# Performance work log

Hardware: AMD Instinct MI355X
Metric: run time of the kernel (lower is better)

## Reference

```python
import jax, jax.numpy as jnp
import numpy as np

NUM_NODES = 8192
IN_FEATURES = 1024
OUT_FEATURES = 512
NUM_EDGES = 262144  # avg degree 32


def setup_inputs() -> dict:
    key = jax.random.key(0)
    k_x, k_w, k_b, k_src, k_dst = jax.random.split(key, 5)
    x = jax.random.normal(k_x, (NUM_NODES, IN_FEATURES), dtype=jnp.float32)
    # torch nn.Linear layout: weight [out, in], bias [out]
    W = jax.random.normal(k_w, (OUT_FEATURES, IN_FEATURES), dtype=jnp.float32) * (1.0 / np.sqrt(IN_FEATURES))
    b = jax.random.normal(k_b, (OUT_FEATURES,), dtype=jnp.float32) * 0.01
    src = jax.random.randint(k_src, (NUM_EDGES,), 0, NUM_NODES, dtype=jnp.int64)
    dst = jax.random.randint(k_dst, (NUM_EDGES,), 0, NUM_NODES, dtype=jnp.int64)
    edge_index = jnp.stack([src, dst], axis=0)
    return {"x": x, "W": W, "b": b, "edge_index": edge_index, "num_nodes": NUM_NODES}


def reference(x, W, b, edge_index, num_nodes):
    # Faithful to the torch module: build dense adjacency from edge list
    # (duplicate edges collapse to 1.0 via assignment semantics),
    # linear, (dropout p=0 -> identity), dense adj @ hidden, relu.
    adj = jnp.zeros((num_nodes, num_nodes), dtype=x.dtype)
    adj = adj.at[edge_index[0], edge_index[1]].set(1.0)
    hidden = x @ W.T + b            # [N, out]
    support = adj @ hidden          # [N, out] aggregation over neighbors
    return jax.nn.relu(support)
```

## Files before the change

kernel.cpp:

```cpp
#include <hip/hip_runtime.h>

#define N_NODES 8192
#define IN_F    1024
#define OUT_F   512
#define N_EDGES 262144
#define STRIDE  96

#define HID_OFF     0u
#define XB_OFF      8388608u
#define WB_OFF      25165824u
#define DEG_OFF     26214400u
#define COL_OFF     26247168u
#define UCNT_OFF    29392896u
#define UCOL_OFF    29425664u
#define MAX_DEG     STRIDE

typedef short  bf16x8 __attribute__((ext_vector_type(8)));
typedef float  f32x4  __attribute__((ext_vector_type(4)));
typedef float  f32x2  __attribute__((ext_vector_type(2)));

__device__ __forceinline__ unsigned short f2bf(float f) {
    unsigned u = __float_as_uint(f);
    u += 0x7fffu + ((u >> 16) & 1u);
    return (unsigned short)(u >> 16);
}

__device__ __forceinline__ float bflo(unsigned u) { return __uint_as_float(u << 16); }
__device__ __forceinline__ float bfhi(unsigned u) { return __uint_as_float(u & 0xffff0000u); }

__device__ __forceinline__ void ld_lds16(const void* g, void* l) {
    __builtin_amdgcn_global_load_lds(
        (const __attribute__((address_space(1))) void*)g,
        (__attribute__((address_space(3))) void*)l, 16, 0, 0);
}

#define NX8 (N_NODES * IN_F / 8)
#define NW8 (OUT_F * IN_F / 8)
__global__ __launch_bounds__(256) void cvt_bf16_all(const float* __restrict__ x,
                                                    const float* __restrict__ w,
                                                    unsigned short* __restrict__ xb,
                                                    int* __restrict__ deg) {
    int i = blockIdx.x * blockDim.x + threadIdx.x;
    if (i < N_NODES) deg[i] = 0;
    if (i >= NX8 + NW8) return;
    const f32x4* p = (i < NX8) ? ((const f32x4*)x + (size_t)i * 2)
                               : ((const f32x4*)w + (size_t)(i - NX8) * 2);
    f32x4 v0 = __builtin_nontemporal_load(p);
    f32x4 v1 = __builtin_nontemporal_load(p + 1);
    uint4 o;
    o.x = (unsigned)f2bf(v0.x) | ((unsigned)f2bf(v0.y) << 16);
    o.y = (unsigned)f2bf(v0.z) | ((unsigned)f2bf(v0.w) << 16);
    o.z = (unsigned)f2bf(v1.x) | ((unsigned)f2bf(v1.y) << 16);
    o.w = (unsigned)f2bf(v1.z) | ((unsigned)f2bf(v1.w) << 16);
    *((uint4*)xb + i) = o;
}

#define GEMM_BLOCKS 512

__global__ __launch_bounds__(256, 2) void gemm_scatter(const unsigned short* __restrict__ Xb,
                                                       const unsigned short* __restrict__ Wb,
                                                       const float* __restrict__ bias,
                                                       unsigned short* __restrict__ H,
                                                       const int* __restrict__ src,
                                                       const int* __restrict__ dst,
                                                       int* __restrict__ deg,
                                                       int* __restrict__ col) {
    __shared__ unsigned short As[2][128 * 64];
    __shared__ unsigned short Bs[2][64 * 64];

    const int bid = blockIdx.x;
    const int tid = threadIdx.x;

    if (bid >= GEMM_BLOCKS) {
        int e = (bid - GEMM_BLOCKS) * 256 + tid;
        int s = src[e];
        int slot = atomicAdd(&deg[s], 1);
        if (slot < STRIDE) col[s * STRIDE + slot] = dst[e];
        return;
    }

    const int lane = tid & 63;
    const int wave = tid >> 6;
    const int row0 = (bid & 63) * 128;
    const int col0 = (bid >> 6) * 64;
    const int wm   = (wave & 1) * 64;
    const int wn   = (wave >> 1) * 32;
    const int fm   = lane & 15;
    const int fm7  = fm & 7;
    const int q    = lane >> 4;

    f32x4 acc[4][2];
#pragma unroll
    for (int i = 0; i < 4; ++i)
#pragma unroll
        for (int j = 0; j < 2; ++j) acc[i][j] = (f32x4)0.f;

    const int r0 = tid >> 3;
    const int kp = ((tid & 7) ^ (r0 & 7)) * 8;
    const unsigned short* Xbase = Xb + (size_t)(row0 + r0) * IN_F + kp;
    const unsigned short* Wbase = Wb + (size_t)(col0 + r0) * IN_F + kp;

#define STAGE(buf, k0) do {                                                   \
    ld_lds16(Xbase            + (k0), &As[buf][tid * 8]);                     \
    ld_lds16(Xbase + 32*IN_F  + (k0), &As[buf][(tid + 256) * 8]);             \
    ld_lds16(Xbase + 64*IN_F  + (k0), &As[buf][(tid + 512) * 8]);             \
    ld_lds16(Xbase + 96*IN_F  + (k0), &As[buf][(tid + 768) * 8]);             \
    ld_lds16(Wbase            + (k0), &Bs[buf][tid * 8]);                     \
    ld_lds16(Wbase + 32*IN_F  + (k0), &Bs[buf][(tid + 256) * 8]);             \
} while (0)

#define COMPUTE(buf) do {                                                     \
    _Pragma("unroll")                                                         \
    for (int s = 0; s < 2; ++s) {                                             \
        const int kq = s * 4 + q;                                             \
        bf16x8 a[4], b[2];                                                    \
        _Pragma("unroll")                                                     \
        for (int mi = 0; mi < 4; ++mi)                                        \
            a[mi] = *(const bf16x8*)&As[buf][(((wm + mi*16 + fm) << 3) + (kq ^ fm7)) << 3]; \
        _Pragma("unroll")                                                     \
        for (int ni = 0; ni < 2; ++ni)                                        \
            b[ni] = *(const bf16x8*)&Bs[buf][(((wn + ni*16 + fm) << 3) + (kq ^ fm7)) << 3]; \
        _Pragma("unroll")                                                     \
        for (int mi = 0; mi < 4; ++mi)                                        \
            _Pragma("unroll")                                                 \
            for (int ni = 0; ni < 2; ++ni)                                    \
                acc[mi][ni] = __builtin_amdgcn_mfma_f32_16x16x32_bf16(        \
                    a[mi], b[ni], acc[mi][ni], 0, 0, 0);                      \
    }                                                                         \
} while (0)

    STAGE(0, 0);
    __syncthreads();
    int cur = 0;
    for (int t = 0; t < 15; ++t) {
        STAGE(cur ^ 1, (t + 1) * 64);
        COMPUTE(cur);
        __syncthreads();
        cur ^= 1;
    }
    COMPUTE(cur);

    const int cm = (lane >> 4) * 4;
#pragma unroll
    for (int ni = 0; ni < 2; ++ni) {
        const int c = col0 + wn + ni * 16 + fm;
        const float bv = bias[c];
#pragma unroll
        for (int mi = 0; mi < 4; ++mi) {
#pragma unroll
            for (int r = 0; r < 4; ++r) {
                const int row = row0 + wm + mi * 16 + cm + r;
                H[(size_t)row * OUT_F + c] = f2bf(acc[mi][ni][r] + bv);
            }
        }
    }
#undef STAGE
#undef COMPUTE
}

__global__ __launch_bounds__(256) void dedup(const int* __restrict__ dg,
                                             const int* __restrict__ col,
                                             int* __restrict__ ucol,
                                             int* __restrict__ ucnt) {
    __shared__ int nbr[4][MAX_DEG];
    __shared__ int wcnt[4];
    const int wave = threadIdx.x >> 6;
    const int lane = threadIdx.x & 63;
    const int v    = blockIdx.x * 4 + wave;
    int d = dg[v];
    if (d > MAX_DEG) d = MAX_DEG;

    if (lane == 0) wcnt[wave] = 0;
    int id0 = -1, id1 = -1;
    if (lane < d)      { id0 = col[v * STRIDE + lane];      nbr[wave][lane]      = id0; }
    if (64 + lane < d) { id1 = col[v * STRIDE + 64 + lane]; nbr[wave][64 + lane] = id1; }
    __builtin_amdgcn_wave_barrier();

    bool k0 = (lane < d);
    const int lim0 = k0 ? lane : 0;
    for (int j = 0; j < lim0; ++j) k0 = k0 & (nbr[wave][j] != id0);
    bool k1 = (64 + lane < d);
    const int lim1 = k1 ? (64 + lane) : 0;
    for (int j = 0; j < lim1; ++j) k1 = k1 & (nbr[wave][j] != id1);
    if (k0) ucol[v * STRIDE + atomicAdd(&wcnt[wave], 1)] = id0;
    if (k1) ucol[v * STRIDE + atomicAdd(&wcnt[wave], 1)] = id1;
    __builtin_amdgcn_wave_barrier();
    if (lane == 0) ucnt[v] = wcnt[wave];
}

__global__ __launch_bounds__(256, 8) void aggregate(const unsigned short* __restrict__ H,
                                                    const int* __restrict__ ucnt,
                                                    const int* __restrict__ ucol,
                                                    float* __restrict__ out) {
    const int wave = threadIdx.x >> 6;
    const int lane = threadIdx.x & 63;
    const int bid  = blockIdx.x;
    const int q    = bid & 3;
    const int v    = (bid >> 2) * 4 + wave;
    const int n    = ucnt[v];
    const int* uq  = ucol + v * STRIDE;
    const unsigned short* Hq = H + q * 128 + lane * 2;

    float a0 = 0.f, a1 = 0.f;
    int e = 0;
    for (; e + 16 <= n; e += 16) {
        unsigned h[16];
#pragma unroll
        for (int t = 0; t < 16; ++t)
            h[t] = *(const unsigned*)&Hq[(size_t)uq[e + t] * OUT_F];
#pragma unroll
        for (int t = 0; t < 16; ++t) { a0 += bflo(h[t]); a1 += bfhi(h[t]); }
    }
    for (; e + 4 <= n; e += 4) {
        unsigned h[4];
#pragma unroll
        for (int t = 0; t < 4; ++t)
            h[t] = *(const unsigned*)&Hq[(size_t)uq[e + t] * OUT_F];
#pragma unroll
        for (int t = 0; t < 4; ++t) { a0 += bflo(h[t]); a1 += bfhi(h[t]); }
    }
    for (; e < n; ++e) {
        unsigned h = *(const unsigned*)&Hq[(size_t)uq[e] * OUT_F];
        a0 += bflo(h); a1 += bfhi(h);
    }
    f32x2 o = {fmaxf(a0, 0.f), fmaxf(a1, 0.f)};
    __builtin_nontemporal_store(o, (f32x2*)&out[(size_t)v * OUT_F + q * 128 + lane * 2]);
}

extern "C" void kernel_launch(void* const* d_in, const int* in_sizes, int n_in,
                              void* d_out, int out_size, void* d_ws, size_t ws_size,
                              hipStream_t stream) {
    const float* x  = (const float*)d_in[0];
    const float* W  = (const float*)d_in[1];
    const float* b  = (const float*)d_in[2];
    const int*   ei = (const int*)d_in[3];
    float* out = (float*)d_out;

    char* ws = (char*)d_ws;
    unsigned short* H    = (unsigned short*)(ws + HID_OFF);
    unsigned short* Xb   = (unsigned short*)(ws + XB_OFF);
    unsigned short* Wb   = (unsigned short*)(ws + WB_OFF);
    int*            deg  = (int*)(ws + DEG_OFF);
    int*            col  = (int*)(ws + COL_OFF);
    int*            ucnt = (int*)(ws + UCNT_OFF);
    int*            ucol = (int*)(ws + UCOL_OFF);

    cvt_bf16_all<<<(NX8 + NW8 + 255) / 256, 256, 0, stream>>>(x, W, Xb, deg);

    gemm_scatter<<<GEMM_BLOCKS + N_EDGES / 256, 256, 0, stream>>>(
        Xb, Wb, b, H, ei, ei + N_EDGES, deg, col);

    dedup<<<N_NODES / 4, 256, 0, stream>>>(deg, col, ucol, ucnt);

    aggregate<<<N_NODES * 4 / 4, 256, 0, stream>>>(H, ucnt, ucol, out);
}
```

Before: 140.6 us.

## Fuse the X fp32-to-bf16 conversion into the GEMM LDS pipeline

Drops the separate pass that converted X to bf16 in global memory. The GEMM now streams fp32 X tiles straight into LDS through a swizzled layout and converts each A fragment to bf16 in registers with v_cvt_pk_bf16_f32 just before the MFMA. This removes a full read of fp32 X plus the write and re-read of the bf16 copy. In exchange, the A tile in LDS doubles in size, the GEMM moves twice as many bytes per X tile, and the conversion is repeated by every wave that shares those rows.

```diff
diff --git a/kernel.cpp b/kernel.cpp
--- a/kernel.cpp
+++ b/kernel.cpp
@@ -7,12 +7,11 @@
 #define STRIDE  96
 
 #define HID_OFF     0u
-#define XB_OFF      8388608u
-#define WB_OFF      25165824u
-#define DEG_OFF     26214400u
-#define COL_OFF     26247168u
-#define UCNT_OFF    29392896u
-#define UCOL_OFF    29425664u
+#define WB_OFF      8388608u
+#define DEG_OFF     9437184u
+#define COL_OFF     9469952u
+#define UCNT_OFF    12615680u
+#define UCOL_OFF    12648448u
 #define MAX_DEG     STRIDE
 
 typedef short  bf16x8 __attribute__((ext_vector_type(8)));
@@ -34,17 +33,13 @@
         (__attribute__((address_space(3))) void*)l, 16, 0, 0);
 }
 
-#define NX8 (N_NODES * IN_F / 8)
 #define NW8 (OUT_F * IN_F / 8)
-__global__ __launch_bounds__(256) void cvt_bf16_all(const float* __restrict__ x,
-                                                    const float* __restrict__ w,
-                                                    unsigned short* __restrict__ xb,
-                                                    int* __restrict__ deg) {
+__global__ __launch_bounds__(256) void cvt_w(const float* __restrict__ w,
+                                             unsigned short* __restrict__ wb,
+                                             int* __restrict__ deg) {
     int i = blockIdx.x * blockDim.x + threadIdx.x;
     if (i < N_NODES) deg[i] = 0;
-    if (i >= NX8 + NW8) return;
-    const f32x4* p = (i < NX8) ? ((const f32x4*)x + (size_t)i * 2)
-                               : ((const f32x4*)w + (size_t)(i - NX8) * 2);
+    const f32x4* p = (const f32x4*)w + (size_t)i * 2;
     f32x4 v0 = __builtin_nontemporal_load(p);
     f32x4 v1 = __builtin_nontemporal_load(p + 1);
     uint4 o;
@@ -52,12 +47,12 @@
     o.y = (unsigned)f2bf(v0.z) | ((unsigned)f2bf(v0.w) << 16);
     o.z = (unsigned)f2bf(v1.x) | ((unsigned)f2bf(v1.y) << 16);
     o.w = (unsigned)f2bf(v1.z) | ((unsigned)f2bf(v1.w) << 16);
-    *((uint4*)xb + i) = o;
+    *((uint4*)wb + i) = o;
 }
 
 #define GEMM_BLOCKS 512
 
-__global__ __launch_bounds__(256, 2) void gemm_scatter(const unsigned short* __restrict__ Xb,
+__global__ __launch_bounds__(256, 2) void gemm_scatter(const float* __restrict__ X,
                                                        const unsigned short* __restrict__ Wb,
                                                        const float* __restrict__ bias,
                                                        unsigned short* __restrict__ H,
@@ -65,7 +60,7 @@
                                                        const int* __restrict__ dst,
                                                        int* __restrict__ deg,
                                                        int* __restrict__ col) {
-    __shared__ unsigned short As[2][128 * 64];
+    __shared__ float          Asf[2][8192];
     __shared__ unsigned short Bs[2][64 * 64];
 
     const int bid = blockIdx.x;
@@ -95,28 +90,41 @@
 #pragma unroll
         for (int j = 0; j < 2; ++j) acc[i][j] = (f32x4)0.f;
 
+    const int acperm = (tid >> 1) & 7;
+    const int ac     = acperm ^ ((tid >> 4) & 7);
+    const float* Xa  = X + (size_t)(row0 + (tid >> 4)) * IN_F + ac * 8 + (tid & 1) * 4;
     const int r0 = tid >> 3;
     const int kp = ((tid & 7) ^ (r0 & 7)) * 8;
-    const unsigned short* Xbase = Xb + (size_t)(row0 + r0) * IN_F + kp;
     const unsigned short* Wbase = Wb + (size_t)(col0 + r0) * IN_F + kp;
 
 #define STAGE(buf, k0) do {                                                   \
-    ld_lds16(Xbase            + (k0), &As[buf][tid * 8]);                     \
-    ld_lds16(Xbase + 32*IN_F  + (k0), &As[buf][(tid + 256) * 8]);             \
-    ld_lds16(Xbase + 64*IN_F  + (k0), &As[buf][(tid + 512) * 8]);             \
-    ld_lds16(Xbase + 96*IN_F  + (k0), &As[buf][(tid + 768) * 8]);             \
+    _Pragma("unroll")                                                         \
+    for (int j = 0; j < 8; ++j)                                               \
+        ld_lds16(Xa + (size_t)j * 16 * IN_F + (k0),                           \
+                 &Asf[buf][(size_t)(j * 256 + tid) * 4]);                     \
     ld_lds16(Wbase            + (k0), &Bs[buf][tid * 8]);                     \
     ld_lds16(Wbase + 32*IN_F  + (k0), &Bs[buf][(tid + 256) * 8]);             \
 } while (0)
 
 #define COMPUTE(buf) do {                                                     \
     _Pragma("unroll")                                                         \
-    for (int s = 0; s < 2; ++s) {                                             \
-        const int kq = s * 4 + q;                                             \
+    for (int s2 = 0; s2 < 2; ++s2) {                                          \
+        const int kq = s2 * 4 + q;                                            \
         bf16x8 a[4], b[2];                                                    \
         _Pragma("unroll")                                                     \
-        for (int mi = 0; mi < 4; ++mi)                                        \
-            a[mi] = *(const bf16x8*)&As[buf][(((wm + mi*16 + fm) << 3) + (kq ^ fm7)) << 3]; \
+        for (int mi = 0; mi < 4; ++mi) {                                      \
+            const int rr = wm + mi * 16 + fm;                                 \
+            const f32x4* pa = (const f32x4*)&Asf[buf][(size_t)(rr * 16 + ((kq ^ fm7) << 1)) * 4]; \
+            f32x4 lo = pa[0], hi = pa[1];                                     \
+            unsigned u0, u1, u2, u3;                                          \
+            asm("v_cvt_pk_bf16_f32 %0, %1, %2" : "=v"(u0) : "v"(lo.x), "v"(lo.y)); \
+            asm("v_cvt_pk_bf16_f32 %0, %1, %2" : "=v"(u1) : "v"(lo.z), "v"(lo.w)); \
+            asm("v_cvt_pk_bf16_f32 %0, %1, %2" : "=v"(u2) : "v"(hi.x), "v"(hi.y)); \
+            asm("v_cvt_pk_bf16_f32 %0, %1, %2" : "=v"(u3) : "v"(hi.z), "v"(hi.w)); \
+            union { unsigned u[4]; bf16x8 v; } pk;                            \
+            pk.u[0] = u0; pk.u[1] = u1; pk.u[2] = u2; pk.u[3] = u3;           \
+            a[mi] = pk.v;                                                     \
+        }                                                                     \
         _Pragma("unroll")                                                     \
         for (int ni = 0; ni < 2; ++ni)                                        \
             b[ni] = *(const bf16x8*)&Bs[buf][(((wn + ni*16 + fm) << 3) + (kq ^ fm7)) << 3]; \
@@ -238,17 +246,16 @@
 
     char* ws = (char*)d_ws;
     unsigned short* H    = (unsigned short*)(ws + HID_OFF);
-    unsigned short* Xb   = (unsigned short*)(ws + XB_OFF);
     unsigned short* Wb   = (unsigned short*)(ws + WB_OFF);
     int*            deg  = (int*)(ws + DEG_OFF);
     int*            col  = (int*)(ws + COL_OFF);
     int*            ucnt = (int*)(ws + UCNT_OFF);
     int*            ucol = (int*)(ws + UCOL_OFF);
 
-    cvt_bf16_all<<<(NX8 + NW8 + 255) / 256, 256, 0, stream>>>(x, W, Xb, deg);
+    cvt_w<<<NW8 / 256, 256, 0, stream>>>(W, Wb, deg);
 
     gemm_scatter<<<GEMM_BLOCKS + N_EDGES / 256, 256, 0, stream>>>(
-        Xb, Wb, b, H, ei, ei + N_EDGES, deg, col);
+        x, Wb, b, H, ei, ei + N_EDGES, deg, col);
 
     dedup<<<N_NODES / 4, 256, 0, stream>>>(deg, col, ucol, ucnt);
 
```

Result: no change. 140.0 us (-0.4%).

## Reschedule graph preprocessing into conversion and GEMM kernels; widen GEMM tile to 128x128

Applied to the files above, without the earlier changes.

The edge scatter moves into the bf16 conversion kernel and the dedup pass moves into the GEMM kernel as extra blocks, with degree zeroing done by a memset. This removes one kernel launch and overlaps graph preprocessing with the dense work. The GEMM tile grows from 128x64 to 128x128, giving 256 blocks with more accumulators each. That raises register and LDS use per block and lowers the block count, which may hurt occupancy and load balance on the GPU's many CUs.

```diff
diff --git a/kernel.cpp b/kernel.cpp
--- a/kernel.cpp
+++ b/kernel.cpp
@@ -36,12 +36,23 @@
 
 #define NX8 (N_NODES * IN_F / 8)
 #define NW8 (OUT_F * IN_F / 8)
-__global__ __launch_bounds__(256) void cvt_bf16_all(const float* __restrict__ x,
-                                                    const float* __restrict__ w,
-                                                    unsigned short* __restrict__ xb,
-                                                    int* __restrict__ deg) {
-    int i = blockIdx.x * blockDim.x + threadIdx.x;
-    if (i < N_NODES) deg[i] = 0;
+#define SCAT_BLOCKS 1024
+__global__ __launch_bounds__(256) void cvt_scatter(const float* __restrict__ x,
+                                                   const float* __restrict__ w,
+                                                   unsigned short* __restrict__ xb,
+                                                   const int* __restrict__ src,
+                                                   const int* __restrict__ dst,
+                                                   int* __restrict__ deg,
+                                                   int* __restrict__ col) {
+    const int bid = blockIdx.x;
+    if (bid < SCAT_BLOCKS) {
+        int e = bid * 256 + threadIdx.x;
+        int s = src[e];
+        int slot = atomicAdd(&deg[s], 1);
+        if (slot < STRIDE) col[s * STRIDE + slot] = dst[e];
+        return;
+    }
+    int i = (bid - SCAT_BLOCKS) * 256 + threadIdx.x;
     if (i >= NX8 + NW8) return;
     const f32x4* p = (i < NX8) ? ((const f32x4*)x + (size_t)i * 2)
                                : ((const f32x4*)w + (size_t)(i - NX8) * 2);
@@ -55,75 +66,96 @@
     *((uint4*)xb + i) = o;
 }
 
-#define GEMM_BLOCKS 512
-
-__global__ __launch_bounds__(256, 2) void gemm_scatter(const unsigned short* __restrict__ Xb,
-                                                       const unsigned short* __restrict__ Wb,
-                                                       const float* __restrict__ bias,
-                                                       unsigned short* __restrict__ H,
-                                                       const int* __restrict__ src,
-                                                       const int* __restrict__ dst,
-                                                       int* __restrict__ deg,
-                                                       int* __restrict__ col) {
+#define GEMM_BLOCKS 256
+
+__global__ __launch_bounds__(256, 2) void gemm_dedup(const unsigned short* __restrict__ Xb,
+                                                     const unsigned short* __restrict__ Wb,
+                                                     const float* __restrict__ bias,
+                                                     unsigned short* __restrict__ H,
+                                                     const int* __restrict__ dg,
+                                                     const int* __restrict__ col,
+                                                     int* __restrict__ ucol,
+                                                     int* __restrict__ ucnt) {
     __shared__ unsigned short As[2][128 * 64];
-    __shared__ unsigned short Bs[2][64 * 64];
+    __shared__ unsigned short Bs[2][128 * 64];
+    __shared__ int wcnt[4];
 
     const int bid = blockIdx.x;
     const int tid = threadIdx.x;
-
-    if (bid >= GEMM_BLOCKS) {
-        int e = (bid - GEMM_BLOCKS) * 256 + tid;
-        int s = src[e];
-        int slot = atomicAdd(&deg[s], 1);
-        if (slot < STRIDE) col[s * STRIDE + slot] = dst[e];
-        return;
-    }
-
     const int lane = tid & 63;
     const int wave = tid >> 6;
+
+    if (bid >= GEMM_BLOCKS) {
+        int* nbr = (int*)&As[0][0];
+        int* mynbr = nbr + wave * MAX_DEG;
+        const int v = (bid - GEMM_BLOCKS) * 4 + wave;
+        int d = dg[v];
+        if (d > MAX_DEG) d = MAX_DEG;
+
+        if (lane == 0) wcnt[wave] = 0;
+        int id0 = -1, id1 = -1;
+        if (lane < d)      { id0 = col[v * STRIDE + lane];      mynbr[lane]      = id0; }
+        if (64 + lane < d) { id1 = col[v * STRIDE + 64 + lane]; mynbr[64 + lane] = id1; }
+        __builtin_amdgcn_wave_barrier();
+
+        bool k0 = (lane < d);
+        const int lim0 = k0 ? lane : 0;
+        for (int j = 0; j < lim0; ++j) k0 = k0 & (mynbr[j] != id0);
+        bool k1 = (64 + lane < d);
+        const int lim1 = k1 ? (64 + lane) : 0;
+        for (int j = 0; j < lim1; ++j) k1 = k1 & (mynbr[j] != id1);
+        if (k0) ucol[v * STRIDE + atomicAdd(&wcnt[wave], 1)] = id0;
+        if (k1) ucol[v * STRIDE + atomicAdd(&wcnt[wave], 1)] = id1;
+        __builtin_amdgcn_wave_barrier();
+        if (lane == 0) ucnt[v] = wcnt[wave];
+        return;
+    }
+
     const int row0 = (bid & 63) * 128;
-    const int col0 = (bid >> 6) * 64;
+    const int col0 = (bid >> 6) * 128;
     const int wm   = (wave & 1) * 64;
-    const int wn   = (wave >> 1) * 32;
+    const int wn   = (wave >> 1) * 64;
     const int fm   = lane & 15;
     const int fm7  = fm & 7;
     const int q    = lane >> 4;
 
-    f32x4 acc[4][2];
+    f32x4 acc[4][4];
 #pragma unroll
     for (int i = 0; i < 4; ++i)
 #pragma unroll
-        for (int j = 0; j < 2; ++j) acc[i][j] = (f32x4)0.f;
+        for (int j = 0; j < 4; ++j) acc[i][j] = (f32x4)0.f;
 
     const int r0 = tid >> 3;
     const int kp = ((tid & 7) ^ (r0 & 7)) * 8;
     const unsigned short* Xbase = Xb + (size_t)(row0 + r0) * IN_F + kp;
     const unsigned short* Wbase = Wb + (size_t)(col0 + r0) * IN_F + kp;
 
-#define STAGE(buf, k0) do {                                                   \
-    ld_lds16(Xbase            + (k0), &As[buf][tid * 8]);                     \
-    ld_lds16(Xbase + 32*IN_F  + (k0), &As[buf][(tid + 256) * 8]);             \
-    ld_lds16(Xbase + 64*IN_F  + (k0), &As[buf][(tid + 512) * 8]);             \
-    ld_lds16(Xbase + 96*IN_F  + (k0), &As[buf][(tid + 768) * 8]);             \
-    ld_lds16(Wbase            + (k0), &Bs[buf][tid * 8]);                     \
-    ld_lds16(Wbase + 32*IN_F  + (k0), &Bs[buf][(tid + 256) * 8]);             \
+#define STAGE(buf, k0s) do {                                                  \
+    ld_lds16(Xbase            + (k0s), &As[buf][tid * 8]);                    \
+    ld_lds16(Xbase + 32*IN_F  + (k0s), &As[buf][(tid + 256) * 8]);            \
+    ld_lds16(Xbase + 64*IN_F  + (k0s), &As[buf][(tid + 512) * 8]);            \
+    ld_lds16(Xbase + 96*IN_F  + (k0s), &As[buf][(tid + 768) * 8]);            \
+    ld_lds16(Wbase            + (k0s), &Bs[buf][tid * 8]);                    \
+    ld_lds16(Wbase + 32*IN_F  + (k0s), &Bs[buf][(tid + 256) * 8]);            \
+    ld_lds16(Wbase + 64*IN_F  + (k0s), &Bs[buf][(tid + 512) * 8]);            \
+    ld_lds16(Wbase + 96*IN_F  + (k0s), &Bs[buf][(tid + 768) * 8]);            \
 } while (0)
 
 #define COMPUTE(buf) do {                                                     \
     _Pragma("unroll")                                                         \
-    for (int s = 0; s < 2; ++s) {                                             \
-        const int kq = s * 4 + q;                                             \
-        bf16x8 a[4], b[2];                                                    \
+    for (int s2 = 0; s2 < 2; ++s2) {                                          \
+        const int kq = s2 * 4 + q;                                            \
+        bf16x8 a[4], b[4];                                                    \
         _Pragma("unroll")                                                     \
         for (int mi = 0; mi < 4; ++mi)                                        \
             a[mi] = *(const bf16x8*)&As[buf][(((wm + mi*16 + fm) << 3) + (kq ^ fm7)) << 3]; \
         _Pragma("unroll")                                                     \
-        for (int ni = 0; ni < 2; ++ni)                                        \
+        for (int ni = 0; ni < 4; ++ni)                                        \
             b[ni] = *(const bf16x8*)&Bs[buf][(((wn + ni*16 + fm) << 3) + (kq ^ fm7)) << 3]; \
         _Pragma("unroll")                                                     \
         for (int mi = 0; mi < 4; ++mi)                                        \
             _Pragma("unroll")                                                 \
-            for (int ni = 0; ni < 2; ++ni)                                    \
+            for (int ni = 0; ni < 4; ++ni)                                    \
                 acc[mi][ni] = __builtin_amdgcn_mfma_f32_16x16x32_bf16(        \
                     a[mi], b[ni], acc[mi][ni], 0, 0, 0);                      \
     }                                                                         \
@@ -142,7 +174,7 @@
 
     const int cm = (lane >> 4) * 4;
 #pragma unroll
-    for (int ni = 0; ni < 2; ++ni) {
+    for (int ni = 0; ni < 4; ++ni) {
         const int c = col0 + wn + ni * 16 + fm;
         const float bv = bias[c];
 #pragma unroll
@@ -156,36 +188,6 @@
     }
 #undef STAGE
 #undef COMPUTE
-}
-
-__global__ __launch_bounds__(256) void dedup(const int* __restrict__ dg,
-                                             const int* __restrict__ col,
-                                             int* __restrict__ ucol,
-                                             int* __restrict__ ucnt) {
-    __shared__ int nbr[4][MAX_DEG];
-    __shared__ int wcnt[4];
-    const int wave = threadIdx.x >> 6;
-    const int lane = threadIdx.x & 63;
-    const int v    = blockIdx.x * 4 + wave;
-    int d = dg[v];
-    if (d > MAX_DEG) d = MAX_DEG;
-
-    if (lane == 0) wcnt[wave] = 0;
-    int id0 = -1, id1 = -1;
-    if (lane < d)      { id0 = col[v * STRIDE + lane];      nbr[wave][lane]      = id0; }
-    if (64 + lane < d) { id1 = col[v * STRIDE + 64 + lane]; nbr[wave][64 + lane] = id1; }
-    __builtin_amdgcn_wave_barrier();
-
-    bool k0 = (lane < d);
-    const int lim0 = k0 ? lane : 0;
-    for (int j = 0; j < lim0; ++j) k0 = k0 & (nbr[wave][j] != id0);
-    bool k1 = (64 + lane < d);
-    const int lim1 = k1 ? (64 + lane) : 0;
-    for (int j = 0; j < lim1; ++j) k1 = k1 & (nbr[wave][j] != id1);
-    if (k0) ucol[v * STRIDE + atomicAdd(&wcnt[wave], 1)] = id0;
-    if (k1) ucol[v * STRIDE + atomicAdd(&wcnt[wave], 1)] = id1;
-    __builtin_amdgcn_wave_barrier();
-    if (lane == 0) ucnt[v] = wcnt[wave];
 }
 
 __global__ __launch_bounds__(256, 8) void aggregate(const unsigned short* __restrict__ H,
@@ -245,12 +247,13 @@
     int*            ucnt = (int*)(ws + UCNT_OFF);
     int*            ucol = (int*)(ws + UCOL_OFF);
 
-    cvt_bf16_all<<<(NX8 + NW8 + 255) / 256, 256, 0, stream>>>(x, W, Xb, deg);
-
-    gemm_scatter<<<GEMM_BLOCKS + N_EDGES / 256, 256, 0, stream>>>(
-        Xb, Wb, b, H, ei, ei + N_EDGES, deg, col);
-
-    dedup<<<N_NODES / 4, 256, 0, stream>>>(deg, col, ucol, ucnt);
+    hipMemsetAsync(deg, 0, N_NODES * sizeof(int), stream);
+
+    cvt_scatter<<<SCAT_BLOCKS + (NX8 + NW8) / 256, 256, 0, stream>>>(
+        x, W, Xb, ei, ei + N_EDGES, deg, col);
+
+    gemm_dedup<<<GEMM_BLOCKS + N_NODES / 4, 256, 0, stream>>>(
+        Xb, Wb, b, H, deg, col, ucol, ucnt);
 
     aggregate<<<N_NODES * 4 / 4, 256, 0, stream>>>(H, ucnt, ucol, out);
 }
```

Measured after the change: 149.4 us. +6.3%, slower.
